# Performance work log

Hardware: AMD Instinct MI355X
Metric: run time of the kernel (lower is better)

## Reference

```python
import jax, jax.numpy as jnp
import numpy as np

N_O = 50000
N_Q = 50000
E = 1_600_000
POS_DIM = 3
LATENT = 128
HEADS = 4
HEAD_DIM = 32
EDGE_IN = 3 * POS_DIM  # ['rel','q_pos','o_pos']


def setup_inputs() -> dict:
    key = jax.random.key(0)
    ks = jax.random.split(key, 12)
    h_obs = jax.random.normal(ks[0], (N_O, LATENT), dtype=jnp.float32)
    pos_obs = jax.random.uniform(ks[1], (N_O, POS_DIM), dtype=jnp.float32)
    pos_query = jax.random.uniform(ks[2], (N_Q, POS_DIM), dtype=jnp.float32)
    src = jax.random.randint(ks[3], (E,), 0, N_O, dtype=jnp.int32)
    dst = jnp.sort(jax.random.randint(ks[4], (E,), 0, N_Q, dtype=jnp.int32))
    s = 0.05
    W1 = jax.random.normal(ks[5], (EDGE_IN, LATENT), dtype=jnp.float32) * s
    b1 = jnp.zeros((LATENT,), dtype=jnp.float32)
    W2 = jax.random.normal(ks[6], (LATENT, HEADS), dtype=jnp.float32) * s
    b2 = jnp.zeros((HEADS,), dtype=jnp.float32)
    Wv = jax.random.normal(ks[7], (LATENT, HEADS * HEAD_DIM), dtype=jnp.float32) * s
    bv = jnp.zeros((HEADS * HEAD_DIM,), dtype=jnp.float32)
    log_sigma = jnp.float32(-2.0)
    return {"h_obs": h_obs, "pos_obs": pos_obs, "pos_query": pos_query,
            "src": src, "dst": dst,
            "W1": W1, "b1": b1, "W2": W2, "b2": b2,
            "Wv": Wv, "bv": bv, "log_sigma": log_sigma}


def _forward(h_obs, pos_obs, pos_query, src, dst, W1, b1, W2, b2, Wv, bv, log_sigma):
    pos_o = pos_obs[src]                      # [E, P]
    pos_q = pos_query[dst]                    # [E, P]
    rel = pos_q - pos_o
    edge_attr = jnp.concatenate([rel, pos_q, pos_o], axis=-1)   # [E, 3P]
    hid = jax.nn.relu(edge_attr @ W1 + b1)                      # [E, LATENT]
    logits = hid @ W2 + b2                                      # [E, H]
    dist2 = jnp.sum(rel * rel, axis=-1, keepdims=True)          # [E, 1]
    sigma = jnp.exp(log_sigma) + 1e-6
    logits = logits - dist2 / (2.0 * sigma * sigma)             # kernel log-weight
    # segment softmax over edges grouped by dst
    n_q = pos_query.shape[0]
    m = jax.ops.segment_max(logits, dst, num_segments=n_q)      # [N_q, H]
    ex = jnp.exp(logits - m[dst])
    denom = jax.ops.segment_sum(ex, dst, num_segments=n_q)      # [N_q, H]
    attn = ex / (denom[dst] + 1e-16)                            # [E, H]
    v = (h_obs @ Wv + bv).reshape(-1, HEADS, HEAD_DIM)          # [N_o, H, D]
    msg = attn[:, :, None] * v[src]                             # [E, H, D]
    out = jax.ops.segment_sum(msg, dst, num_segments=n_q)       # [N_q, H, D]
    return out.reshape(n_q, HEADS * HEAD_DIM)


def reference(h_obs, pos_obs, pos_query, src, dst, W1, b1, W2, b2, Wv, bv, log_sigma):
    return _forward(h_obs, pos_obs, pos_query, src, dst, W1, b1, W2, b2, Wv, bv, log_sigma)
```

## Files before the change

### kernel.cpp

```cpp
#include <hip/hip_runtime.h>
#include <hip/hip_bf16.h>
#include <cstdint>
#include <cstddef>

#define N_O 50000
#define N_Q 50000
#define NE  1600000

#define EDGE_BLOCKS  (NE / 64)
#define VP_BLOCKS    ((N_O + 31) / 32)
#define RP_BLOCKS    ((N_Q + 128) / 128)
#define WCAP 264

typedef __attribute__((ext_vector_type(8)))  short short8;
typedef __attribute__((ext_vector_type(16))) float f32x16;

__device__ inline unsigned short f2bf(float x) {
    __hip_bfloat16 hb = __float2bfloat16(x);
    return *reinterpret_cast<unsigned short*>(&hb);
}

__global__ void pack_kernel(const float* __restrict__ W1, const float* __restrict__ b1,
                            const float* __restrict__ W2, const float* __restrict__ b2,
                            const float* __restrict__ log_sigma,
                            unsigned short* __restrict__ W1cT,
                            unsigned short* __restrict__ W2tb,
                            float* __restrict__ scal) {
    int j = threadIdx.x;
    if (j < 128) {
        #pragma unroll
        for (int a = 0; a < 3; ++a) {
            W1cT[j * 8 + a]     = f2bf(W1[(3 + a) * 128 + j] + W1[a * 128 + j]);
            W1cT[j * 8 + 3 + a] = f2bf(W1[(6 + a) * 128 + j] - W1[a * 128 + j]);
        }
        W1cT[j * 8 + 6] = f2bf(b1[j]);
        W1cT[j * 8 + 7] = 0;
        #pragma unroll
        for (int hd = 0; hd < 4; ++hd)
            W2tb[hd * 128 + j] = f2bf(W2[j * 4 + hd]);
    } else if (j == 128) {
        float sigma = expf(log_sigma[0]) + 1e-6f;
        scal[0] = 1.0f / (2.0f * sigma * sigma);
        scal[1] = b2[0]; scal[2] = b2[1]; scal[3] = b2[2]; scal[4] = b2[3];
    }
}

__device__ void rowptr_body(int bid, const int* __restrict__ dst, int* __restrict__ rp) {
    int q = bid * 128 + threadIdx.x;
    if (q > N_Q) return;
    int lo = 0, hi = NE;
    while (lo < hi) {
        int mid = (lo + hi) >> 1;
        if (dst[mid] < q) lo = mid + 1; else hi = mid;
    }
    rp[q] = lo;
}

__device__ void vproj_body(int bid, const float* __restrict__ h,
                           const float* __restrict__ Wv,
                           const float* __restrict__ bv,
                           unsigned short* __restrict__ v,
                           float* Ash ) {
    int t = threadIdx.x;
    int n0 = bid * 32;
    #pragma unroll
    for (int rep = 0; rep < 8; ++rep) {
        int idx = rep * 128 + t;
        int row = idx >> 5, c4 = (idx & 31) * 4;
        float4 val = make_float4(0.f, 0.f, 0.f, 0.f);
        if (n0 + row < N_O) val = *(const float4*)(h + (size_t)(n0 + row) * 128 + c4);
        float* d = &Ash[row * 132 + c4];
        d[0] = val.x; d[1] = val.y; d[2] = val.z; d[3] = val.w;
    }
    __syncthreads();

    int cg = t & 15, rg = t >> 4;
    int c0 = cg * 8, r0 = rg * 4;
    float acc[4][8];
    #pragma unroll
    for (int i = 0; i < 4; ++i)
        #pragma unroll
        for (int j = 0; j < 8; ++j) acc[i][j] = 0.f;

    const float4* Wv4 = (const float4*)Wv;
    for (int k = 0; k < 128; ++k) {
        float4 b0 = Wv4[k * 32 + cg * 2];
        float4 b1v = Wv4[k * 32 + cg * 2 + 1];
        float bb[8] = {b0.x, b0.y, b0.z, b0.w, b1v.x, b1v.y, b1v.z, b1v.w};
        #pragma unroll
        for (int i = 0; i < 4; ++i) {
            float a = Ash[(r0 + i) * 132 + k];
            #pragma unroll
            for (int j = 0; j < 8; ++j) acc[i][j] += a * bb[j];
        }
    }

    float bvv[8];
    #pragma unroll
    for (int j = 0; j < 8; ++j) bvv[j] = bv[c0 + j];
    #pragma unroll
    for (int i = 0; i < 4; ++i) {
        int n = n0 + r0 + i;
        if (n < N_O) {
            uint4 o;
            __hip_bfloat162 t0 = __float22bfloat162_rn(
                make_float2(acc[i][0] + bvv[0], acc[i][1] + bvv[1]));
            __hip_bfloat162 t1 = __float22bfloat162_rn(
                make_float2(acc[i][2] + bvv[2], acc[i][3] + bvv[3]));
            __hip_bfloat162 t2 = __float22bfloat162_rn(
                make_float2(acc[i][4] + bvv[4], acc[i][5] + bvv[5]));
            __hip_bfloat162 t3 = __float22bfloat162_rn(
                make_float2(acc[i][6] + bvv[6], acc[i][7] + bvv[7]));
            o.x = *reinterpret_cast<unsigned int*>(&t0);
            o.y = *reinterpret_cast<unsigned int*>(&t1);
            o.z = *reinterpret_cast<unsigned int*>(&t2);
            o.w = *reinterpret_cast<unsigned int*>(&t3);
            *(uint4*)(v + (size_t)n * 128 + c0) = o;
        }
    }
}

__device__ void edge_body(int bid, const float* __restrict__ pos_obs,
                          const float* __restrict__ pos_query,
                          const int* __restrict__ src, const int* __restrict__ dst,
                          const unsigned short* __restrict__ W1cT,
                          const unsigned short* __restrict__ W2tb,
                          const float* __restrict__ scal,
                          float* __restrict__ logitsT,
                          unsigned char* smem ) {
    int t = threadIdx.x;
    int wave = t >> 6, lane = t & 63;
    int i = lane & 31, h = lane >> 5;
    unsigned char* myrow = smem + wave * 8448 + i * 264;

    short8 zero8;
    #pragma unroll
    for (int k = 0; k < 8; ++k) zero8[k] = 0;

    short8 a1[4];
    #pragma unroll
    for (int b = 0; b < 4; ++b)
        a1[b] = (h == 0) ? *(const short8*)(W1cT + (32 * b + i) * 8) : zero8;

    short8 a2[8];
    #pragma unroll
    for (int m = 0; m < 8; ++m)
        a2[m] = (i < 4) ? *(const short8*)(W2tb + i * 128 + m * 16 + h * 8) : zero8;

    int e = bid * 64 + wave * 32 + i;
    int s = src[e], d = dst[e];
    float pox = pos_obs[s * 3 + 0], poy = pos_obs[s * 3 + 1], poz = pos_obs[s * 3 + 2];
    float pqx = pos_query[d * 3 + 0], pqy = pos_query[d * 3 + 1], pqz = pos_query[d * 3 + 2];
    float rx = pqx - pox, ry = pqy - poy, rz = pqz - poz;
    float dist2 = rx * rx + ry * ry + rz * rz;

    short8 bea = zero8;
    if (h == 0) {
        bea[0] = (short)f2bf(pqx); bea[1] = (short)f2bf(pqy); bea[2] = (short)f2bf(pqz);
        bea[3] = (short)f2bf(pox); bea[4] = (short)f2bf(poy); bea[5] = (short)f2bf(poz);
        bea[6] = (short)0x3F80;
        bea[7] = 0;
    }

    f32x16 c1[4];
    #pragma unroll
    for (int b = 0; b < 4; ++b) {
        #pragma unroll
        for (int k = 0; k < 16; ++k) c1[b][k] = 0.0f;
        c1[b] = __builtin_amdgcn_mfma_f32_32x32x16_bf16(a1[b], bea, c1[b], 0, 0, 0);
    }

    #pragma unroll
    for (int b = 0; b < 4; ++b) {
        #pragma unroll
        for (int s_ = 0; s_ < 4; ++s_) {
            float x0 = fmaxf(c1[b][4 * s_ + 0], 0.f);
            float x1 = fmaxf(c1[b][4 * s_ + 1], 0.f);
            float x2 = fmaxf(c1[b][4 * s_ + 2], 0.f);
            float x3 = fmaxf(c1[b][4 * s_ + 3], 0.f);
            __hip_bfloat162 p0 = __float22bfloat162_rn(make_float2(x0, x1));
            __hip_bfloat162 p1 = __float22bfloat162_rn(make_float2(x2, x3));
            uint2 w;
            w.x = *reinterpret_cast<unsigned int*>(&p0);
            w.y = *reinterpret_cast<unsigned int*>(&p1);
            *(uint2*)(myrow + 64 * b + 16 * s_ + 8 * h) = w;
        }
    }

    f32x16 c2;
    #pragma unroll
    for (int k = 0; k < 16; ++k) c2[k] = 0.0f;
    #pragma unroll
    for (int m = 0; m < 8; ++m) {
        uint2 lo = *(const uint2*)(myrow + 32 * m + 16 * h);
        uint2 hi = *(const uint2*)(myrow + 32 * m + 16 * h + 8);
        union { unsigned int u[4]; short8 s; } bf;
        bf.u[0] = lo.x; bf.u[1] = lo.y; bf.u[2] = hi.x; bf.u[3] = hi.y;
        c2 = __builtin_amdgcn_mfma_f32_32x32x16_bf16(a2[m], bf.s, c2, 0, 0, 0);
    }

    if (h == 0) {
        float pen = dist2 * scal[0];
        logitsT[0 * NE + e] = c2[0] + scal[1] - pen;
        logitsT[1 * NE + e] = c2[1] + scal[2] - pen;
        logitsT[2 * NE + e] = c2[2] + scal[3] - pen;
        logitsT[3 * NE + e] = c2[3] + scal[4] - pen;
    }
}

__global__ __launch_bounds__(128) void fused_kernel(
        const float* __restrict__ pos_obs, const float* __restrict__ pos_query,
        const int* __restrict__ src, const int* __restrict__ dst,
        const unsigned short* __restrict__ W1cT,
        const unsigned short* __restrict__ W2tb,
        const float* __restrict__ scal, float* __restrict__ logitsT,
        const float* __restrict__ h_obs, const float* __restrict__ Wv,
        const float* __restrict__ bv, unsigned short* __restrict__ vbuf,
        int* __restrict__ rp) {
    __shared__ __align__(16) unsigned char smem[16896];
    int b = blockIdx.x;
    if (b < EDGE_BLOCKS) {
        edge_body(b, pos_obs, pos_query, src, dst, W1cT, W2tb, scal, logitsT, smem);
    } else if (b < EDGE_BLOCKS + VP_BLOCKS) {
        vproj_body(b - EDGE_BLOCKS, h_obs, Wv, bv, vbuf, (float*)smem);
    } else {
        rowptr_body(b - EDGE_BLOCKS - VP_BLOCKS, dst, rp);
    }
}

__global__ __launch_bounds__(256) void attn_kernel(const __hip_bfloat162* __restrict__ vb,
                                                   const float* __restrict__ logitsT,
                                                   const int* __restrict__ src,
                                                   const int* __restrict__ rp,
                                                   float* __restrict__ out) {
    __shared__ __align__(16) float wsh[4 * 4 * WCAP];
    int t = threadIdx.x;
    int lane = t & 63, wave = t >> 6;
    int q = blockIdx.x * 4 + wave;
    int s0 = rp[q], s1 = rp[q + 1];
    int cnt = s1 - s0;
    int h = lane >> 4, i = lane & 15;
    const float* lp = logitsT + (size_t)h * NE;

    float m = -INFINITY;
    for (int e = s0 + i; e < s1; e += 16) m = fmaxf(m, lp[e]);
    #pragma unroll
    for (int off = 8; off; off >>= 1) m = fmaxf(m, __shfl_xor(m, off));

    float acc0 = 0.f, acc1 = 0.f, r;

    if (cnt <= 256) {
        int s0a = s0 & ~3;
        float* wpb = wsh + wave * (4 * WCAP) + h * WCAP;
        float sum = 0.f;
        for (int e = s0 + i; e < s1; e += 16) {
            float w = __expf(lp[e] - m);
            wpb[e - s0a] = w;
            sum += w;
        }
        #pragma unroll
        for (int off = 8; off; off >>= 1) sum += __shfl_xor(sum, off);
        r = 1.0f / (sum + 1e-16f);

        int e = s0;
        int e1 = (s0 + 3) & ~3; if (e1 > s1) e1 = s1;
        for (; e < e1; ++e) {
            float w = wpb[e - s0a];
            float2 f = __bfloat1622float2(vb[(size_t)src[e] * 64 + lane]);
            acc0 += w * f.x; acc1 += w * f.y;
        }
        for (; e + 4 <= s1; e += 4) {
            float4 w4 = *(const float4*)(wpb + (e - s0a));
            int4 s4 = *(const int4*)(src + e);
            float2 f0 = __bfloat1622float2(vb[(size_t)s4.x * 64 + lane]);
            float2 f1 = __bfloat1622float2(vb[(size_t)s4.y * 64 + lane]);
            float2 f2 = __bfloat1622float2(vb[(size_t)s4.z * 64 + lane]);
            float2 f3 = __bfloat1622float2(vb[(size_t)s4.w * 64 + lane]);
            acc0 += w4.x * f0.x + w4.y * f1.x + w4.z * f2.x + w4.w * f3.x;
            acc1 += w4.x * f0.y + w4.y * f1.y + w4.z * f2.y + w4.w * f3.y;
        }
        for (; e < s1; ++e) {
            float w = wpb[e - s0a];
            float2 f = __bfloat1622float2(vb[(size_t)src[e] * 64 + lane]);
            acc0 += w * f.x; acc1 += w * f.y;
        }
    } else {
        float sum = 0.f;
        for (int e = s0 + i; e < s1; e += 16) sum += __expf(lp[e] - m);
        #pragma unroll
        for (int off = 8; off; off >>= 1) sum += __shfl_xor(sum, off);
        r = 1.0f / (sum + 1e-16f);

        int e = s0;
        for (; e < s1 && (e & 3); ++e) {
            float w = __expf(lp[e] - m);
            float2 f = __bfloat1622float2(vb[(size_t)src[e] * 64 + lane]);
            acc0 += w * f.x; acc1 += w * f.y;
        }
        for (; e + 4 <= s1; e += 4) {
            float4 l4 = *(const float4*)(lp + e);
            int4 s4 = *(const int4*)(src + e);
            float w0 = __expf(l4.x - m);
            float w1 = __expf(l4.y - m);
            float w2 = __expf(l4.z - m);
            float w3 = __expf(l4.w - m);
            float2 f0 = __bfloat1622float2(vb[(size_t)s4.x * 64 + lane]);
            float2 f1 = __bfloat1622float2(vb[(size_t)s4.y * 64 + lane]);
            float2 f2 = __bfloat1622float2(vb[(size_t)s4.z * 64 + lane]);
            float2 f3 = __bfloat1622float2(vb[(size_t)s4.w * 64 + lane]);
            acc0 += w0 * f0.x + w1 * f1.x + w2 * f2.x + w3 * f3.x;
            acc1 += w0 * f0.y + w1 * f1.y + w2 * f2.y + w3 * f3.y;
        }
        for (; e < s1; ++e) {
            float w = __expf(lp[e] - m);
            float2 f = __bfloat1622float2(vb[(size_t)src[e] * 64 + lane]);
            acc0 += w * f.x; acc1 += w * f.y;
        }
    }
    *(float2*)(out + (size_t)q * 128 + lane * 2) = make_float2(acc0 * r, acc1 * r);
}

extern "C" void kernel_launch(void* const* d_in, const int* in_sizes, int n_in,
                              void* d_out, int out_size, void* d_ws, size_t ws_size,
                              hipStream_t stream) {
    const float* h_obs     = (const float*)d_in[0];
    const float* pos_obs   = (const float*)d_in[1];
    const float* pos_query = (const float*)d_in[2];
    const int*   src       = (const int*)d_in[3];
    const int*   dst       = (const int*)d_in[4];
    const float* W1        = (const float*)d_in[5];
    const float* b1        = (const float*)d_in[6];
    const float* W2        = (const float*)d_in[7];
    const float* b2        = (const float*)d_in[8];
    const float* Wv        = (const float*)d_in[9];
    const float* bv        = (const float*)d_in[10];
    const float* log_sigma = (const float*)d_in[11];
    float* out = (float*)d_out;

    char* ws = (char*)d_ws;
    int*            rp      = (int*)(ws + 0);
    float*          scal    = (float*)(ws + 200192);
    unsigned short* W1cT    = (unsigned short*)(ws + 200256);
    unsigned short* W2tb    = (unsigned short*)(ws + 202304);
    unsigned short* vbuf    = (unsigned short*)(ws + 208640);
    float*          logitsT = (float*)(ws + 13008768);

    hipLaunchKernelGGL(pack_kernel, dim3(1), dim3(256), 0, stream,
                       W1, b1, W2, b2, log_sigma, W1cT, W2tb, scal);
    hipLaunchKernelGGL(fused_kernel, dim3(EDGE_BLOCKS + VP_BLOCKS + RP_BLOCKS),
                       dim3(128), 0, stream,
                       pos_obs, pos_query, src, dst, W1cT, W2tb, scal, logitsT,
                       h_obs, Wv, bv, vbuf, rp);
    hipLaunchKernelGGL(attn_kernel, dim3(N_Q / 4), dim3(256), 0, stream,
                       (const __hip_bfloat162*)vbuf, logitsT, src, rp, out);
}
```

Measured before the change: 251.9 us.

## Move V projection to split-bf16 MFMA and drop LDS staging in edge MLP

The V projection moves from a scalar FP32 FMA loop with LDS staging to MFMA bf16 matrix ops. Both weights and activations are split into hi/lo bf16 parts and three MFMAs are used per chunk to keep near-FP32 accuracy, with one wave per 32-row tile. The edge MLP no longer round-trips the hidden layer through shared memory: it swaps halves between lanes with cross-lane shuffles and feeds the second MFMA directly. This removes the kernel's shared-memory allocation, which may raise occupancy, at the cost of extra VALU packing work and repeated global loads of Wv.

Result: slower. 285.7 us (+13.5%).

```diff
diff --git a/kernel.cpp b/kernel.cpp
--- a/kernel.cpp
+++ b/kernel.cpp
@@ -8,7 +8,8 @@
 #define NE  1600000
 
 #define EDGE_BLOCKS  (NE / 64)
-#define VP_BLOCKS    ((N_O + 31) / 32)
+#define VP_TILES     ((N_O + 31) / 32)
+#define VP_BLOCKS    ((VP_TILES + 1) / 2)
 #define RP_BLOCKS    ((N_Q + 128) / 128)
 #define WCAP 264
 
@@ -18,6 +19,11 @@
 __device__ inline unsigned short f2bf(float x) {
     __hip_bfloat16 hb = __float2bfloat16(x);
     return *reinterpret_cast<unsigned short*>(&hb);
+}
+
+__device__ inline unsigned pk2(float a, float b) {
+    __hip_bfloat162 t = __float22bfloat162_rn(make_float2(a, b));
+    return *reinterpret_cast<unsigned*>(&t);
 }
 
 __global__ void pack_kernel(const float* __restrict__ W1, const float* __restrict__ b1,
@@ -56,66 +62,78 @@
     rp[q] = lo;
 }
 
-__device__ void vproj_body(int bid, const float* __restrict__ h,
+__device__ void vproj_body(int tile, const float* __restrict__ h,
                            const float* __restrict__ Wv,
                            const float* __restrict__ bv,
-                           unsigned short* __restrict__ v,
-                           float* Ash ) {
-    int t = threadIdx.x;
-    int n0 = bid * 32;
-    #pragma unroll
-    for (int rep = 0; rep < 8; ++rep) {
-        int idx = rep * 128 + t;
-        int row = idx >> 5, c4 = (idx & 31) * 4;
-        float4 val = make_float4(0.f, 0.f, 0.f, 0.f);
-        if (n0 + row < N_O) val = *(const float4*)(h + (size_t)(n0 + row) * 128 + c4);
-        float* d = &Ash[row * 132 + c4];
-        d[0] = val.x; d[1] = val.y; d[2] = val.z; d[3] = val.w;
-    }
-    __syncthreads();
-
-    int cg = t & 15, rg = t >> 4;
-    int c0 = cg * 8, r0 = rg * 4;
-    float acc[4][8];
-    #pragma unroll
-    for (int i = 0; i < 4; ++i)
-        #pragma unroll
-        for (int j = 0; j < 8; ++j) acc[i][j] = 0.f;
-
-    const float4* Wv4 = (const float4*)Wv;
-    for (int k = 0; k < 128; ++k) {
-        float4 b0 = Wv4[k * 32 + cg * 2];
-        float4 b1v = Wv4[k * 32 + cg * 2 + 1];
-        float bb[8] = {b0.x, b0.y, b0.z, b0.w, b1v.x, b1v.y, b1v.z, b1v.w};
-        #pragma unroll
-        for (int i = 0; i < 4; ++i) {
-            float a = Ash[(r0 + i) * 132 + k];
-            #pragma unroll
-            for (int j = 0; j < 8; ++j) acc[i][j] += a * bb[j];
-        }
-    }
-
-    float bvv[8];
-    #pragma unroll
-    for (int j = 0; j < 8; ++j) bvv[j] = bv[c0 + j];
-    #pragma unroll
-    for (int i = 0; i < 4; ++i) {
-        int n = n0 + r0 + i;
-        if (n < N_O) {
-            uint4 o;
-            __hip_bfloat162 t0 = __float22bfloat162_rn(
-                make_float2(acc[i][0] + bvv[0], acc[i][1] + bvv[1]));
-            __hip_bfloat162 t1 = __float22bfloat162_rn(
-                make_float2(acc[i][2] + bvv[2], acc[i][3] + bvv[3]));
-            __hip_bfloat162 t2 = __float22bfloat162_rn(
-                make_float2(acc[i][4] + bvv[4], acc[i][5] + bvv[5]));
-            __hip_bfloat162 t3 = __float22bfloat162_rn(
-                make_float2(acc[i][6] + bvv[6], acc[i][7] + bvv[7]));
-            o.x = *reinterpret_cast<unsigned int*>(&t0);
-            o.y = *reinterpret_cast<unsigned int*>(&t1);
-            o.z = *reinterpret_cast<unsigned int*>(&t2);
-            o.w = *reinterpret_cast<unsigned int*>(&t3);
-            *(uint4*)(v + (size_t)n * 128 + c0) = o;
+                           unsigned short* __restrict__ v) {
+    int lane = threadIdx.x & 63;
+    int i = lane & 31, g = lane >> 5;
+    int n = tile * 32 + i;
+    bool nok = (n < N_O);
+    const float* hrow = h + (size_t)n * 128;
+
+    short8 bh[8];
+    #pragma unroll
+    for (int m = 0; m < 8; ++m) {
+        float4 u0 = make_float4(0.f, 0.f, 0.f, 0.f), u1 = u0;
+        if (nok) {
+            u0 = *(const float4*)(hrow + 16 * m + 8 * g);
+            u1 = *(const float4*)(hrow + 16 * m + 8 * g + 4);
+        }
+        union { unsigned u[4]; short8 s; } p;
+        p.u[0] = pk2(u0.x, u0.y); p.u[1] = pk2(u0.z, u0.w);
+        p.u[2] = pk2(u1.x, u1.y); p.u[3] = pk2(u1.z, u1.w);
+        bh[m] = p.s;
+    }
+
+    #pragma unroll 1
+    for (int c = 0; c < 4; ++c) {
+        f32x16 acc;
+        #pragma unroll
+        for (int k = 0; k < 16; ++k) acc[k] = 0.f;
+        #pragma unroll
+        for (int m = 0; m < 8; ++m) {
+            const float* wp = Wv + (size_t)(16 * m + 8 * g) * 128 + 32 * c + i;
+            float w[8];
+            #pragma unroll
+            for (int j = 0; j < 8; ++j) w[j] = wp[(size_t)j * 128];
+            union { unsigned u[4]; short8 s; } wh, wl, hl;
+            #pragma unroll
+            for (int j = 0; j < 4; ++j) wh.u[j] = pk2(w[2 * j], w[2 * j + 1]);
+            #pragma unroll
+            for (int j = 0; j < 4; ++j) {
+                float e0 = w[2 * j]     - __uint_as_float(wh.u[j] << 16);
+                float e1 = w[2 * j + 1] - __uint_as_float(wh.u[j] & 0xffff0000u);
+                wl.u[j] = pk2(e0, e1);
+            }
+            float4 u0 = make_float4(0.f, 0.f, 0.f, 0.f), u1 = u0;
+            if (nok) {
+                u0 = *(const float4*)(hrow + 16 * m + 8 * g);
+                u1 = *(const float4*)(hrow + 16 * m + 8 * g + 4);
+            }
+            float x[8] = {u0.x, u0.y, u0.z, u0.w, u1.x, u1.y, u1.z, u1.w};
+            union { unsigned u[4]; short8 s; } bhp;
+            bhp.s = bh[m];
+            #pragma unroll
+            for (int j = 0; j < 4; ++j) {
+                float e0 = x[2 * j]     - __uint_as_float(bhp.u[j] << 16);
+                float e1 = x[2 * j + 1] - __uint_as_float(bhp.u[j] & 0xffff0000u);
+                hl.u[j] = pk2(e0, e1);
+            }
+            acc = __builtin_amdgcn_mfma_f32_32x32x16_bf16(wh.s, bh[m], acc, 0, 0, 0);
+            acc = __builtin_amdgcn_mfma_f32_32x32x16_bf16(wh.s, hl.s,  acc, 0, 0, 0);
+            acc = __builtin_amdgcn_mfma_f32_32x32x16_bf16(wl.s, bh[m], acc, 0, 0, 0);
+        }
+        if (nok) {
+            #pragma unroll
+            for (int q = 0; q < 4; ++q) {
+                int vc = 32 * c + 8 * q + 4 * g;
+                float4 bq = *(const float4*)(bv + vc);
+                uint2 ov;
+                ov.x = pk2(acc[4 * q + 0] + bq.x, acc[4 * q + 1] + bq.y);
+                ov.y = pk2(acc[4 * q + 2] + bq.z, acc[4 * q + 3] + bq.w);
+                *(uint2*)(v + (size_t)n * 128 + vc) = ov;
+            }
         }
     }
 }
@@ -126,26 +144,14 @@
                           const unsigned short* __restrict__ W1cT,
                           const unsigned short* __restrict__ W2tb,
                           const float* __restrict__ scal,
-                          float* __restrict__ logitsT,
-                          unsigned char* smem ) {
+                          float* __restrict__ logitsT) {
     int t = threadIdx.x;
     int wave = t >> 6, lane = t & 63;
     int i = lane & 31, h = lane >> 5;
-    unsigned char* myrow = smem + wave * 8448 + i * 264;
 
     short8 zero8;
     #pragma unroll
     for (int k = 0; k < 8; ++k) zero8[k] = 0;
-
-    short8 a1[4];
-    #pragma unroll
-    for (int b = 0; b < 4; ++b)
-        a1[b] = (h == 0) ? *(const short8*)(W1cT + (32 * b + i) * 8) : zero8;
-
-    short8 a2[8];
-    #pragma unroll
-    for (int m = 0; m < 8; ++m)
-        a2[m] = (i < 4) ? *(const short8*)(W2tb + i * 128 + m * 16 + h * 8) : zero8;
 
     int e = bid * 64 + wave * 32 + i;
     int s = src[e], d = dst[e];
@@ -162,41 +168,45 @@
         bea[7] = 0;
     }
 
-    f32x16 c1[4];
+    f32x16 c2;
+    #pragma unroll
+    for (int k = 0; k < 16; ++k) c2[k] = 0.f;
+
     #pragma unroll
     for (int b = 0; b < 4; ++b) {
-        #pragma unroll
-        for (int k = 0; k < 16; ++k) c1[b][k] = 0.0f;
-        c1[b] = __builtin_amdgcn_mfma_f32_32x32x16_bf16(a1[b], bea, c1[b], 0, 0, 0);
-    }
-
-    #pragma unroll
-    for (int b = 0; b < 4; ++b) {
-        #pragma unroll
-        for (int s_ = 0; s_ < 4; ++s_) {
-            float x0 = fmaxf(c1[b][4 * s_ + 0], 0.f);
-            float x1 = fmaxf(c1[b][4 * s_ + 1], 0.f);
-            float x2 = fmaxf(c1[b][4 * s_ + 2], 0.f);
-            float x3 = fmaxf(c1[b][4 * s_ + 3], 0.f);
-            __hip_bfloat162 p0 = __float22bfloat162_rn(make_float2(x0, x1));
-            __hip_bfloat162 p1 = __float22bfloat162_rn(make_float2(x2, x3));
-            uint2 w;
-            w.x = *reinterpret_cast<unsigned int*>(&p0);
-            w.y = *reinterpret_cast<unsigned int*>(&p1);
-            *(uint2*)(myrow + 64 * b + 16 * s_ + 8 * h) = w;
-        }
-    }
-
-    f32x16 c2;
-    #pragma unroll
-    for (int k = 0; k < 16; ++k) c2[k] = 0.0f;
-    #pragma unroll
-    for (int m = 0; m < 8; ++m) {
-        uint2 lo = *(const uint2*)(myrow + 32 * m + 16 * h);
-        uint2 hi = *(const uint2*)(myrow + 32 * m + 16 * h + 8);
-        union { unsigned int u[4]; short8 s; } bf;
-        bf.u[0] = lo.x; bf.u[1] = lo.y; bf.u[2] = hi.x; bf.u[3] = hi.y;
-        c2 = __builtin_amdgcn_mfma_f32_32x32x16_bf16(a2[m], bf.s, c2, 0, 0, 0);
+        short8 a1b = (h == 0) ? *(const short8*)(W1cT + (32 * b + i) * 8) : zero8;
+        f32x16 c1;
+        #pragma unroll
+        for (int k = 0; k < 16; ++k) c1[k] = 0.f;
+        c1 = __builtin_amdgcn_mfma_f32_32x32x16_bf16(a1b, bea, c1, 0, 0, 0);
+
+        unsigned hw[4][2], pw[4][2];
+        #pragma unroll
+        for (int q = 0; q < 4; ++q) {
+            float x0 = fmaxf(c1[4 * q + 0], 0.f);
+            float x1 = fmaxf(c1[4 * q + 1], 0.f);
+            float x2 = fmaxf(c1[4 * q + 2], 0.f);
+            float x3 = fmaxf(c1[4 * q + 3], 0.f);
+            hw[q][0] = pk2(x0, x1);
+            hw[q][1] = pk2(x2, x3);
+        }
+        #pragma unroll
+        for (int q = 0; q < 4; ++q) {
+            pw[q][0] = (unsigned)__shfl_xor((int)hw[q][0], 32);
+            pw[q][1] = (unsigned)__shfl_xor((int)hw[q][1], 32);
+        }
+        #pragma unroll
+        for (int mo = 0; mo < 2; ++mo) {
+            int m = 2 * b + mo;
+            int q0 = 2 * mo, q1 = 2 * mo + 1;
+            short8 a2m = (i < 4) ? *(const short8*)(W2tb + i * 128 + m * 16 + h * 8) : zero8;
+            union { unsigned u[4]; short8 s8; } bf;
+            bf.u[0] = h ? pw[q1][0] : hw[q0][0];
+            bf.u[1] = h ? pw[q1][1] : hw[q0][1];
+            bf.u[2] = h ? hw[q1][0] : pw[q0][0];
+            bf.u[3] = h ? hw[q1][1] : pw[q0][1];
+            c2 = __builtin_amdgcn_mfma_f32_32x32x16_bf16(a2m, bf.s8, c2, 0, 0, 0);
+        }
     }
 
     if (h == 0) {
@@ -217,12 +227,12 @@
         const float* __restrict__ h_obs, const float* __restrict__ Wv,
         const float* __restrict__ bv, unsigned short* __restrict__ vbuf,
         int* __restrict__ rp) {
-    __shared__ __align__(16) unsigned char smem[16896];
     int b = blockIdx.x;
     if (b < EDGE_BLOCKS) {
-        edge_body(b, pos_obs, pos_query, src, dst, W1cT, W2tb, scal, logitsT, smem);
+        edge_body(b, pos_obs, pos_query, src, dst, W1cT, W2tb, scal, logitsT);
     } else if (b < EDGE_BLOCKS + VP_BLOCKS) {
-        vproj_body(b - EDGE_BLOCKS, h_obs, Wv, bv, vbuf, (float*)smem);
+        int tile = (b - EDGE_BLOCKS) * 2 + (threadIdx.x >> 6);
+        if (tile < VP_TILES) vproj_body(tile, h_obs, Wv, bv, vbuf);
     } else {
         rowptr_body(b - EDGE_BLOCKS - VP_BLOCKS, dst, rp);
     }
```
